# Performance work log

Measured on AMD Instinct MI355X. Metric: run time of the kernel, lower is better.

## Reference

```python
import jax, jax.numpy as jnp
import numpy as np

N_EMBD = 1024
N_HEAD = 16
B, T = 2, 2048


def setup_inputs() -> dict:
    key = jax.random.key(0)
    ks = jax.random.split(key, 9)
    s = 1.0 / np.sqrt(N_EMBD)
    return {
        "x": jax.random.normal(ks[0], (B, T, N_EMBD), dtype=jnp.float32),
        "Wq": jax.random.normal(ks[1], (N_EMBD, N_EMBD), dtype=jnp.float32) * s,
        "bq": jax.random.normal(ks[2], (N_EMBD,), dtype=jnp.float32) * s,
        "Wk": jax.random.normal(ks[3], (N_EMBD, N_EMBD), dtype=jnp.float32) * s,
        "bk": jax.random.normal(ks[4], (N_EMBD,), dtype=jnp.float32) * s,
        "Wv": jax.random.normal(ks[5], (N_EMBD, N_EMBD), dtype=jnp.float32) * s,
        "bv": jax.random.normal(ks[6], (N_EMBD,), dtype=jnp.float32) * s,
        "Wp": jax.random.normal(ks[7], (N_EMBD, N_EMBD), dtype=jnp.float32) * s,
        "bp": jax.random.normal(ks[8], (N_EMBD,), dtype=jnp.float32) * s,
    }


def reference(x, Wq, bq, Wk, bk, Wv, bv, Wp, bp):
    b, t, c = x.shape
    hd = c // N_HEAD  # head dim
    # torch Linear: x @ W.T + b; reshape to (B, H, T, hd)
    def heads(W, bias):
        return (x @ W.T + bias).reshape(b, t, N_HEAD, hd).transpose(0, 2, 1, 3)
    q, k, v = heads(Wq, bq), heads(Wk, bk), heads(Wv, bv)
    scale = 1.0 / np.sqrt(hd)
    att = jnp.einsum("bhqd,bhkd->bhqk", q, k) * scale  # (B,H,T,T)
    causal = jnp.tril(jnp.ones((t, t), dtype=bool))
    att = jnp.where(causal[None, None], att, -jnp.inf)
    att = jax.nn.softmax(att, axis=-1)
    y = jnp.einsum("bhqk,bhkd->bhqd", att, v)
    y = y.transpose(0, 2, 1, 3).reshape(b, t, c)
    return y @ Wp.T + bp
```

## Files before the change

### kernel.cpp

```cpp
#include <hip/hip_runtime.h>

typedef __bf16 bf16x8 __attribute__((ext_vector_type(8)));
typedef __bf16 bf16x4 __attribute__((ext_vector_type(4)));
typedef float f32x4 __attribute__((ext_vector_type(4)));

#define DEVI __device__ __forceinline__

constexpr int NE = 1024;
constexpr int NH = 16;
constexpr int HD = 64;
constexpr int BB = 2;
constexpr int TT = 2048;
constexpr int MM = BB * TT;

DEVI unsigned short f2bf(float f) {
  union { float f; unsigned u; } v; v.f = f;
  unsigned r = v.u + 0x7FFFu + ((v.u >> 16) & 1u);
  return (unsigned short)(r >> 16);
}

__global__ __launch_bounds__(256) void cvt_bf16(const float* __restrict__ in,
                                                unsigned short* __restrict__ out, int n4) {
  int i = blockIdx.x * blockDim.x + threadIdx.x;
  if (i >= n4) return;
  float4 v = reinterpret_cast<const float4*>(in)[i];
  ushort4 o;
  o.x = f2bf(v.x); o.y = f2bf(v.y); o.z = f2bf(v.z); o.w = f2bf(v.w);
  reinterpret_cast<ushort4*>(out)[i] = o;
}

__global__ __launch_bounds__(256) void cvt_w(const float* __restrict__ q, const float* __restrict__ k,
                                             const float* __restrict__ v, const float* __restrict__ p,
                                             unsigned short* __restrict__ out) {
  int i = blockIdx.x * blockDim.x + threadIdx.x;
  const int seg = i >> 18;
  const float* src = (seg == 0) ? q : (seg == 1) ? k : (seg == 2) ? v : p;
  float4 vv = reinterpret_cast<const float4*>(src)[i & 0x3FFFF];
  ushort4 o;
  o.x = f2bf(vv.x); o.y = f2bf(vv.y); o.z = f2bf(vv.z); o.w = f2bf(vv.w);
  reinterpret_cast<ushort4*>(out)[i] = o;
}

template <int BM, int MODE>
__global__ __launch_bounds__(256)
void gemm_nt(const unsigned short* __restrict__ A, const unsigned short* __restrict__ Bm,
             const float* __restrict__ b0, const float* __restrict__ b1, const float* __restrict__ b2,
             void* __restrict__ o0, unsigned short* __restrict__ o1, unsigned short* __restrict__ o2,
             int K, int nbx) {
  constexpr int WAVES_N = (BM == 128) ? 2 : 4;
  constexpr int NJ = (BM == 128) ? 4 : 2;
  constexpr int A_LPW = BM / 64;
  __shared__ __align__(16) unsigned short As[BM * 32];
  __shared__ __align__(16) unsigned short Bs[128 * 32];
  const int tid = threadIdx.x;
  const int wid = tid >> 6;
  const int lane = tid & 63;
  const int l15 = lane & 15, l4 = lane >> 4;

  const int id = blockIdx.x;
  const int chunk = gridDim.x >> 3;
  const int idp = (id & 7) * chunk + (id >> 3);
  const int bx = idp / (gridDim.x / nbx), by = idp % (gridDim.x / nbx);

  const int brow = by * BM;
  const int bcol = bx * 128;
  const int wm = wid / WAVES_N, wn = wid % WAVES_N;
  const int wmoff = wm * 64;
  const int wnoff = wn * (128 / WAVES_N);

  f32x4 acc[4][NJ] = {};

  const int srow = lane >> 2;
  const int scol = (lane & 3) * 8;

  for (int kb = 0; kb < K; kb += 32) {
#pragma unroll
    for (int c = 0; c < A_LPW; ++c) {
      const int rb = wid * (BM / 4) + c * 16;
      __builtin_amdgcn_global_load_lds(
          (const __attribute__((address_space(1))) void*)(A + (size_t)(brow + rb + srow) * K + kb + scol),
          (__attribute__((address_space(3))) void*)&As[rb * 32], 16, 0, 0);
    }
#pragma unroll
    for (int c = 0; c < 2; ++c) {
      const int rb = wid * 32 + c * 16;
      __builtin_amdgcn_global_load_lds(
          (const __attribute__((address_space(1))) void*)(Bm + (size_t)(bcol + rb + srow) * K + kb + scol),
          (__attribute__((address_space(3))) void*)&Bs[rb * 32], 16, 0, 0);
    }
    __syncthreads();

    bf16x8 af[4], bfj[NJ];
#pragma unroll
    for (int i = 0; i < 4; ++i)
      af[i] = *reinterpret_cast<const bf16x8*>(&As[(wmoff + i * 16 + l15) * 32 + l4 * 8]);
#pragma unroll
    for (int j = 0; j < NJ; ++j)
      bfj[j] = *reinterpret_cast<const bf16x8*>(&Bs[(wnoff + j * 16 + l15) * 32 + l4 * 8]);
#pragma unroll
    for (int i = 0; i < 4; ++i)
#pragma unroll
      for (int j = 0; j < NJ; ++j)
        acc[i][j] = __builtin_amdgcn_mfma_f32_16x16x32_bf16(af[i], bfj[j], acc[i][j], 0, 0, 0);
    __syncthreads();
  }

  if (MODE == 0) {
#pragma unroll
    for (int j = 0; j < NJ; ++j) {
      const int col = bcol + wnoff + j * 16 + l15;
      const float bv = b0[col];
#pragma unroll
      for (int i = 0; i < 4; ++i) {
        const int row0 = brow + wmoff + i * 16 + l4 * 4;
#pragma unroll
        for (int r = 0; r < 4; ++r)
          ((float*)o0)[(size_t)(row0 + r) * NE + col] = acc[i][j][r] + bv;
      }
    }
  } else {
    const int seg = bcol >> 10;
    const float* bsel = (seg == 0) ? b0 : (seg == 1) ? b1 : b2;
    unsigned short* qk = (seg == 0) ? (unsigned short*)o0 : o1;
#pragma unroll
    for (int j = 0; j < NJ; ++j) {
      const int col = bcol + wnoff + j * 16 + l15;
      const int dcol = col & 1023;
      const int h = dcol >> 6, d = dcol & 63;
      const float bv = bsel[dcol];
#pragma unroll
      for (int i = 0; i < 4; ++i) {
        const int row0 = brow + wmoff + i * 16 + l4 * 4;
#pragma unroll
        for (int r = 0; r < 4; ++r) {
          const int row = row0 + r;
          const int b = row >> 11, t = row & (TT - 1);
          const unsigned short val = f2bf(acc[i][j][r] + bv);
          if (seg < 2)
            qk[((size_t)((b * NH + h) * TT + t) << 6) + d] = val;
          else
            o2[((size_t)(b * NH + h) * HD + d) * TT + t] = val;
        }
      }
    }
  }
}

__global__ __launch_bounds__(256, 3)
void attn(const unsigned short* __restrict__ Q, const unsigned short* __restrict__ Kk,
          const unsigned short* __restrict__ Vt, unsigned short* __restrict__ Y) {
  __shared__ __align__(16) unsigned short Ks[2][64 * 64];
  __shared__ __align__(16) unsigned short Vs[2][64 * 64];
  __shared__ __align__(16) unsigned short Pw[4][32 * 64];
  const int tid = threadIdx.x, wid = tid >> 6, lane = tid & 63;
  const int l15 = lane & 15, l4 = lane >> 4;

  const int id = blockIdx.x;
  const int j = id & 255, kk = id >> 8;
  const int bh = (j & 15) + 16 * kk;
  const int xt = kk ? 15 - (j >> 4) : (j >> 4);

  const int qb0 = xt * 128;
  const int qw = qb0 + wid * 32;
  const unsigned short* Qh = Q + (size_t)bh * TT * HD;
  const unsigned short* Kh = Kk + (size_t)bh * TT * HD;
  const unsigned short* Vh = Vt + (size_t)bh * HD * TT;

  bf16x8 qf[2][2];
#pragma unroll
  for (int qt = 0; qt < 2; ++qt)
#pragma unroll
    for (int ks = 0; ks < 2; ++ks) {
      bf16x8 t = *reinterpret_cast<const bf16x8*>(&Qh[(qw + qt * 16 + l15) * 64 + ks * 32 + l4 * 8]);
#pragma unroll
      for (int e = 0; e < 8; ++e) t[e] = (__bf16)((float)t[e] * 0.125f);
      qf[qt][ks] = t;
    }

  float m_[2] = {-3e38f, -3e38f};
  float l_[2] = {0.f, 0.f};
  f32x4 accO[4][2] = {};

  const int srow8 = lane >> 3;
  const int scol8 = lane & 7;
  const int nkb = 2 * (xt + 1);

  auto stage = [&](int buf, int kb) {
#pragma unroll
    for (int c = 0; c < 2; ++c) {
      const int row = (wid * 2 + c) * 8 + srow8;
      const int sc = (scol8 ^ (row & 7)) * 8;
      __builtin_amdgcn_global_load_lds(
          (const __attribute__((address_space(1))) void*)(Kh + (size_t)(kb + row) * 64 + sc),
          (__attribute__((address_space(3))) void*)&Ks[buf][(wid * 2 + c) * 512], 16, 0, 0);
      __builtin_amdgcn_global_load_lds(
          (const __attribute__((address_space(1))) void*)(Vh + (size_t)row * TT + kb + sc),
          (__attribute__((address_space(3))) void*)&Vs[buf][(wid * 2 + c) * 512], 16, 0, 0);
    }
  };

  stage(0, 0);
  int cur = 0;
  for (int kbi = 0; kbi < nkb; ++kbi) {
    const int kb = kbi * 64;
    __syncthreads();
    if (kbi + 1 < nkb) stage(cur ^ 1, kb + 64);

    if (kb < qw + 32) {
      const bool diag = (kb + 63 > qw);
      const char* ksb = (const char*)Ks[cur];
      const char* vsb = (const char*)Vs[cur];
      char* pwb = (char*)&Pw[wid][0];

      f32x4 z[4][2];
#pragma unroll
      for (int kt = 0; kt < 4; ++kt) {
        const int row = kt * 16 + l15;
        bf16x8 kf0 = *reinterpret_cast<const bf16x8*>(ksb + row * 128 + (((0 + l4) ^ (row & 7)) << 4));
        bf16x8 kf1 = *reinterpret_cast<const bf16x8*>(ksb + row * 128 + (((4 + l4) ^ (row & 7)) << 4));
#pragma unroll
        for (int qt = 0; qt < 2; ++qt) {
          f32x4 zz = {};
          zz = __builtin_amdgcn_mfma_f32_16x16x32_bf16(kf0, qf[qt][0], zz, 0, 0, 0);
          zz = __builtin_amdgcn_mfma_f32_16x16x32_bf16(kf1, qf[qt][1], zz, 0, 0, 0);
          z[kt][qt] = zz;
        }
      }

      if (diag) {
#pragma unroll
        for (int kt = 0; kt < 4; ++kt)
#pragma unroll
          for (int qt = 0; qt < 2; ++qt)
#pragma unroll
            for (int r = 0; r < 4; ++r) {
              const int key = kb + kt * 16 + l4 * 4 + r;
              const int qi = qw + qt * 16 + l15;
              z[kt][qt][r] = (key <= qi) ? z[kt][qt][r] : -3e38f;
            }
      }

#pragma unroll
      for (int qt = 0; qt < 2; ++qt) {
        float tm[8];
#pragma unroll
        for (int i = 0; i < 8; ++i)
          tm[i] = fmaxf(z[(2 * i) >> 2][qt][(2 * i) & 3], z[(2 * i + 1) >> 2][qt][(2 * i + 1) & 3]);
#pragma unroll
        for (int i = 0; i < 4; ++i) tm[i] = fmaxf(tm[i], tm[i + 4]);
        float pm = fmaxf(fmaxf(tm[0], tm[2]), fmaxf(tm[1], tm[3]));
        pm = fmaxf(pm, __shfl_xor(pm, 16, 64));
        pm = fmaxf(pm, __shfl_xor(pm, 32, 64));

        if (!__all(pm <= m_[qt] + 8.f)) {
          const float mn = fmaxf(m_[qt], pm);
          const float sf = __expf(m_[qt] - mn);
          m_[qt] = mn;
          l_[qt] *= sf;
#pragma unroll
          for (int dt = 0; dt < 4; ++dt)
#pragma unroll
            for (int r = 0; r < 4; ++r) accO[dt][qt][r] *= sf;
        }

#pragma unroll
        for (int kt = 0; kt < 4; ++kt)
#pragma unroll
          for (int r = 0; r < 4; ++r)
            z[kt][qt][r] = __expf(z[kt][qt][r] - m_[qt]);
        float ts[8];
#pragma unroll
        for (int i = 0; i < 8; ++i)
          ts[i] = z[(2 * i) >> 2][qt][(2 * i) & 3] + z[(2 * i + 1) >> 2][qt][(2 * i + 1) & 3];
#pragma unroll
        for (int i = 0; i < 4; ++i) ts[i] += ts[i + 4];
        float rs = (ts[0] + ts[2]) + (ts[1] + ts[3]);
        rs += __shfl_xor(rs, 16, 64);
        rs += __shfl_xor(rs, 32, 64);
        l_[qt] += rs;

        const int q = qt * 16 + l15;
#pragma unroll
        for (int kt = 0; kt < 4; ++kt) {
          bf16x4 pk;
#pragma unroll
          for (int r = 0; r < 4; ++r) pk[r] = (__bf16)z[kt][qt][r];
          const int c16 = kt * 2 + (l4 >> 1);
          *reinterpret_cast<bf16x4*>(pwb + q * 128 + ((c16 ^ (q & 7)) << 4) + (l4 & 1) * 8) = pk;
        }
      }

      asm volatile("s_waitcnt lgkmcnt(0)" ::: "memory");
      __builtin_amdgcn_sched_barrier(0);

#pragma unroll
      for (int ks = 0; ks < 2; ++ks) {
        bf16x8 pb[2];
#pragma unroll
        for (int qt = 0; qt < 2; ++qt) {
          const int q = qt * 16 + l15;
          pb[qt] = *reinterpret_cast<const bf16x8*>(pwb + q * 128 + ((((ks << 2) + l4) ^ (q & 7)) << 4));
        }
#pragma unroll
        for (int dt = 0; dt < 4; ++dt) {
          const int row = dt * 16 + l15;
          bf16x8 vf = *reinterpret_cast<const bf16x8*>(vsb + row * 128 + ((((ks << 2) + l4) ^ (row & 7)) << 4));
#pragma unroll
          for (int qt = 0; qt < 2; ++qt)
            accO[dt][qt] = __builtin_amdgcn_mfma_f32_16x16x32_bf16(vf, pb[qt], accO[dt][qt], 0, 0, 0);
        }
      }
    }
    cur ^= 1;
  }

  const int b = bh >> 4, h = bh & 15;
#pragma unroll
  for (int qt = 0; qt < 2; ++qt) {
    const float inv = 1.0f / l_[qt];
    const int q = qw + qt * 16 + l15;
#pragma unroll
    for (int dt = 0; dt < 4; ++dt) {
      bf16x4 o;
#pragma unroll
      for (int r = 0; r < 4; ++r) o[r] = (__bf16)(accO[dt][qt][r] * inv);
      *reinterpret_cast<bf16x4*>(&Y[((size_t)(b * TT + q)) * NE + h * 64 + dt * 16 + l4 * 4]) = o;
    }
  }
}

extern "C" void kernel_launch(void* const* d_in, const int* in_sizes, int n_in,
                              void* d_out, int out_size, void* d_ws, size_t ws_size,
                              hipStream_t stream) {
  const float* x  = (const float*)d_in[0];
  const float* Wq = (const float*)d_in[1];
  const float* bq = (const float*)d_in[2];
  const float* Wk = (const float*)d_in[3];
  const float* bk = (const float*)d_in[4];
  const float* Wv = (const float*)d_in[5];
  const float* bv = (const float*)d_in[6];
  const float* Wp = (const float*)d_in[7];
  const float* bp = (const float*)d_in[8];

  char* ws = (char*)d_ws;
  const size_t MB = 1u << 20;
  unsigned short* xb   = (unsigned short*)(ws + 0 * MB);
  unsigned short* Wqkv = (unsigned short*)(ws + 8 * MB);
  unsigned short* Wpb  = (unsigned short*)(ws + 14 * MB);
  unsigned short* Qb   = (unsigned short*)(ws + 16 * MB);
  unsigned short* Kb   = (unsigned short*)(ws + 24 * MB);
  unsigned short* Vtb  = (unsigned short*)(ws + 32 * MB);
  unsigned short* yb   = (unsigned short*)(ws + 40 * MB);

  cvt_bf16<<<MM * NE / 4 / 256, 256, 0, stream>>>(x, xb, MM * NE / 4);
  cvt_w<<<4 * NE * NE / 4 / 256, 256, 0, stream>>>(Wq, Wk, Wv, Wp, Wqkv);

  gemm_nt<128, 1><<<768, 256, 0, stream>>>(xb, Wqkv, bq, bk, bv, Qb, Kb, Vtb, NE, 24);

  attn<<<512, 256, 0, stream>>>(Qb, Kb, Vtb, yb);

  gemm_nt<64, 0><<<512, 256, 0, stream>>>(yb, Wpb, bp, nullptr, nullptr, d_out, nullptr, nullptr, NE, 8);
}
```

Before: 227.0 us.

## Triple-buffer GEMM LDS tiles with async prefetch and XOR-swizzled layout

```diff
diff --git a/kernel.cpp b/kernel.cpp
--- a/kernel.cpp
+++ b/kernel.cpp
@@ -42,7 +42,7 @@
 }
 
 template <int BM, int MODE>
-__global__ __launch_bounds__(256)
+__global__ __launch_bounds__(256, (BM == 128) ? 3 : 2)
 void gemm_nt(const unsigned short* __restrict__ A, const unsigned short* __restrict__ Bm,
              const float* __restrict__ b0, const float* __restrict__ b1, const float* __restrict__ b2,
              void* __restrict__ o0, unsigned short* __restrict__ o1, unsigned short* __restrict__ o2,
@@ -50,8 +50,8 @@
   constexpr int WAVES_N = (BM == 128) ? 2 : 4;
   constexpr int NJ = (BM == 128) ? 4 : 2;
   constexpr int A_LPW = BM / 64;
-  __shared__ __align__(16) unsigned short As[BM * 32];
-  __shared__ __align__(16) unsigned short Bs[128 * 32];
+  __shared__ __align__(16) unsigned short As[3][BM * 32];
+  __shared__ __align__(16) unsigned short Bs[3][128 * 32];
   const int tid = threadIdx.x;
   const int wid = tid >> 6;
   const int lane = tid & 63;
@@ -71,39 +71,66 @@
   f32x4 acc[4][NJ] = {};
 
   const int srow = lane >> 2;
-  const int scol = (lane & 3) * 8;
-
-  for (int kb = 0; kb < K; kb += 32) {
+  const int sscol = ((lane & 3) ^ ((lane >> 3) & 3)) * 8;
+
+  auto stage = [&](int buf, int t) {
+    const int kb = t * 32;
 #pragma unroll
     for (int c = 0; c < A_LPW; ++c) {
       const int rb = wid * (BM / 4) + c * 16;
       __builtin_amdgcn_global_load_lds(
-          (const __attribute__((address_space(1))) void*)(A + (size_t)(brow + rb + srow) * K + kb + scol),
-          (__attribute__((address_space(3))) void*)&As[rb * 32], 16, 0, 0);
+          (const __attribute__((address_space(1))) void*)(A + (size_t)(brow + rb + srow) * K + kb + sscol),
+          (__attribute__((address_space(3))) void*)&As[buf][rb * 32], 16, 0, 0);
     }
 #pragma unroll
     for (int c = 0; c < 2; ++c) {
       const int rb = wid * 32 + c * 16;
       __builtin_amdgcn_global_load_lds(
-          (const __attribute__((address_space(1))) void*)(Bm + (size_t)(bcol + rb + srow) * K + kb + scol),
-          (__attribute__((address_space(3))) void*)&Bs[rb * 32], 16, 0, 0);
-    }
-    __syncthreads();
-
+          (const __attribute__((address_space(1))) void*)(Bm + (size_t)(bcol + rb + srow) * K + kb + sscol),
+          (__attribute__((address_space(3))) void*)&Bs[buf][rb * 32], 16, 0, 0);
+    }
+  };
+
+  const int roff = l15 * 32 + (l4 ^ ((l15 >> 1) & 3)) * 8;
+
+  auto compute = [&](int cb) {
     bf16x8 af[4], bfj[NJ];
 #pragma unroll
     for (int i = 0; i < 4; ++i)
-      af[i] = *reinterpret_cast<const bf16x8*>(&As[(wmoff + i * 16 + l15) * 32 + l4 * 8]);
+      af[i] = *reinterpret_cast<const bf16x8*>(&As[cb][(wmoff + i * 16) * 32 + roff]);
 #pragma unroll
     for (int j = 0; j < NJ; ++j)
-      bfj[j] = *reinterpret_cast<const bf16x8*>(&Bs[(wnoff + j * 16 + l15) * 32 + l4 * 8]);
+      bfj[j] = *reinterpret_cast<const bf16x8*>(&Bs[cb][(wnoff + j * 16) * 32 + roff]);
 #pragma unroll
     for (int i = 0; i < 4; ++i)
 #pragma unroll
       for (int j = 0; j < NJ; ++j)
         acc[i][j] = __builtin_amdgcn_mfma_f32_16x16x32_bf16(af[i], bfj[j], acc[i][j], 0, 0, 0);
-    __syncthreads();
+  };
+
+  const int NT = K / 32;
+  stage(0, 0);
+  stage(1, 1);
+  int cb = 0, sb = 2;
+  for (int t = 0; t + 2 < NT; ++t) {
+    stage(sb, t + 2);
+    if constexpr (BM == 128) asm volatile("s_waitcnt vmcnt(8)" ::: "memory");
+    else                     asm volatile("s_waitcnt vmcnt(6)" ::: "memory");
+    asm volatile("s_barrier" ::: "memory");
+    compute(cb);
+    asm volatile("s_barrier" ::: "memory");
+    sb = cb;
+    cb = (cb == 2) ? 0 : cb + 1;
   }
+  if constexpr (BM == 128) asm volatile("s_waitcnt vmcnt(4)" ::: "memory");
+  else                     asm volatile("s_waitcnt vmcnt(3)" ::: "memory");
+  asm volatile("s_barrier" ::: "memory");
+  compute(cb);
+  asm volatile("s_barrier" ::: "memory");
+  cb = (cb == 2) ? 0 : cb + 1;
+  asm volatile("s_waitcnt vmcnt(0)" ::: "memory");
+  asm volatile("s_barrier" ::: "memory");
+  compute(cb);
 
   if (MODE == 0) {
 #pragma unroll
```

New measurement: 215.9 us. -4.9%, faster.
